# Kernel optimization log

Hardware: AMD Instinct MI355X
Metric: run time of the kernel (lower is better)

Reference implementation:

```python
import jax, jax.numpy as jnp
import numpy as np

# --- configuration (matches init_kwargs / input_specs) ---
B = 8            # point clouds per batch
N_PER = 4096     # points per cloud
RATIO = 0.25
M_PER = int(N_PER * RATIO)
K = 64           # max_num_neighbors (hard-coded in source)
R = 0.2          # ball-query radius
C_IN = 64
DIMS = [C_IN + 3, 128, 128, 256]  # local_nn MLP dims (x_j || pos_j - pos_i)


def setup_inputs() -> dict:
    key = jax.random.key(0)
    ks = jax.random.split(key, 8)
    N = B * N_PER
    x = jax.random.normal(ks[0], (N, C_IN), jnp.float32)
    pos = jax.random.uniform(ks[1], (N, 3), jnp.float32)   # unit cube -> r=0.2 meaningful
    batch = jnp.repeat(jnp.arange(B), N_PER)               # sorted cloud ids
    params = {}
    for i, (din, dout) in enumerate(zip(DIMS[:-1], DIMS[1:])):
        params[f"W{i+1}"] = jax.random.normal(ks[2 + i], (din, dout), jnp.float32) / np.sqrt(din)
        params[f"b{i+1}"] = jnp.zeros((dout,), jnp.float32)
    return {"x": x, "pos": pos, "batch": batch, **params}


def _fps(pos, m):
    """Farthest point sampling on one cloud. pos: [n,3] -> [m] int32 indices.
    Deterministic start at index 0 (torch_geometric uses a random start)."""
    n = pos.shape[0]

    def step(carry, _):
        d, cur = carry
        dist = jnp.sum((pos - pos[cur]) ** 2, axis=-1)
        d = jnp.minimum(d, dist)
        nxt = jnp.argmax(d).astype(jnp.int32)
        return (d, nxt), cur

    init = (jnp.full((n,), jnp.inf, pos.dtype), jnp.int32(0))
    (_, _), idx = jax.lax.scan(step, init, None, length=m)
    return idx  # [m]


def _sa_one(x, pos, W1, b1, W2, b2, W3, b3):
    """One cloud: fps -> radius ball query (<=K nearest within R) -> PointConv (max aggr)."""
    idx = _fps(pos, M_PER)                 # [m]
    q = pos[idx]                           # [m,3] centroids
    d2 = jnp.sum((q[:, None, :] - pos[None, :, :]) ** 2, axis=-1)  # [m,n]
    negd, nbr = jax.lax.top_k(-d2, K)      # K nearest candidates per centroid
    valid = (-negd) <= R * R               # inside the radius ball (self always valid)
    rel = pos[nbr] - q[:, None, :]         # [m,K,3]  pos_j - pos_i
    h = jnp.concatenate([x[nbr], rel], axis=-1)   # [m,K,C+3]
    h = jax.nn.relu(h @ W1 + b1)
    h = jax.nn.relu(h @ W2 + b2)
    h = jax.nn.relu(h @ W3 + b3)           # [m,K,256]
    h = jnp.where(valid[..., None], h, -jnp.inf)
    out = jnp.max(h, axis=1)               # max aggregation over neighbors
    out = jnp.where(jnp.any(valid, axis=1)[..., None], out, 0.0)
    return out, idx


def reference(x, pos, batch, W1, b1, W2, b2, W3, b3):
    xb = x.reshape(B, N_PER, C_IN)
    pb = pos.reshape(B, N_PER, 3)
    out, idx = jax.vmap(lambda xc, pc: _sa_one(xc, pc, W1, b1, W2, b2, W3, b3))(xb, pb)
    pos_out = jnp.take_along_axis(pb, idx[..., None], axis=1).reshape(B * M_PER, 3)
    batch_out = jnp.repeat(jnp.arange(B), M_PER)
    return out.reshape(B * M_PER, DIMS[-1]), pos_out, batch_out
```

## Files before the change

### kernel.cpp

```cpp
#include <hip/hip_runtime.h>


#define NB 8
#define NP 4096
#define MP 1024
#define NC 8192
#define CIN 64
#define D1 128
#define D2 128
#define D3 256
#define CAP 512

static constexpr float R2F = 0.04f;

typedef _Float16 f16;
typedef _Float16 half8 __attribute__((ext_vector_type(8)));
typedef float floatx4 __attribute__((ext_vector_type(4)));
typedef unsigned long long u64;

#define OUT1 ((size_t)NC * D3)
#define OUT2 (OUT1 + (size_t)NC * 3)

template<int CTRL>
__device__ __forceinline__ float dppmax(float v) {
  const int iv = __builtin_bit_cast(int, v);
  const int sh = __builtin_amdgcn_update_dpp(iv, iv, CTRL, 0xf, 0xf, false);
  return fmaxf(v, __builtin_bit_cast(float, sh));
}

struct FpsS { float ldspos[NP * 3]; u64 pkey[2][4]; int cidx[MP]; };
struct PkS  { float wl[CIN * D1]; float xl[32 * CIN]; };

__launch_bounds__(256)
__global__ void front_kernel(const float* __restrict__ pos, const float* __restrict__ x,
                             const float* __restrict__ W1, const float* __restrict__ b1,
                             const float* __restrict__ W2, const float* __restrict__ W3,
                             float* __restrict__ qpos, f16* __restrict__ P,
                             f16* __restrict__ W2t, f16* __restrict__ W3t,
                             float* __restrict__ W1b, float* __restrict__ dout) {
  __shared__ __align__(16) char raw[sizeof(FpsS)];
  const int bid = blockIdx.x;
  const int t = threadIdx.x;

  if (bid < NB) {
    FpsS& S = *reinterpret_cast<FpsS*>(raw);
    const int b = bid;
    const int lane = t & 63, wv = t >> 6;
    for (int e = t; e < NP * 3; e += 256) S.ldspos[e] = pos[(size_t)b * NP * 3 + e];
    __syncthreads();
    float px[16], py[16], pz[16], d[16];
    #pragma unroll
    for (int i = 0; i < 16; ++i) {
      const int p = t * 16 + i;
      px[i] = S.ldspos[p * 3 + 0]; py[i] = S.ldspos[p * 3 + 1]; pz[i] = S.ldspos[p * 3 + 2];
      d[i] = INFINITY;
    }
    int g = 0;
    for (int step = 0; step < MP; ++step) {
      if (t == 0) S.cidx[step] = g;
      const float cx = S.ldspos[g * 3 + 0], cy = S.ldspos[g * 3 + 1], cz = S.ldspos[g * 3 + 2];
      float lv = -1.0f;
      #pragma unroll
      for (int i = 0; i < 16; ++i) {
        const float dx = __fsub_rn(px[i], cx);
        const float dy = __fsub_rn(py[i], cy);
        const float dz = __fsub_rn(pz[i], cz);
        const float nd = __fadd_rn(__fadd_rn(__fmul_rn(dx, dx), __fmul_rn(dy, dy)),
                                   __fmul_rn(dz, dz));
        d[i] = fminf(d[i], nd);
        lv = fmaxf(lv, d[i]);
      }
      int li = 15;
      #pragma unroll
      for (int i = 14; i >= 0; --i) li = (d[i] == lv) ? i : li;
      float wm = lv;
      wm = dppmax<0xB1>(wm);
      wm = dppmax<0x4E>(wm);
      wm = dppmax<0x141>(wm);
      wm = dppmax<0x140>(wm);
      wm = dppmax<0x142>(wm);
      wm = dppmax<0x143>(wm);
      const float M = __builtin_bit_cast(float,
          __builtin_amdgcn_readlane(__builtin_bit_cast(int, wm), 63));
      const u64 bal = __ballot(lv == M);
      const int Ls = (int)__builtin_ctzll(bal);
      const int sli = __builtin_amdgcn_readlane(li, Ls);
      const int gw = ((wv << 6) + Ls) * 16 + sli;
      if (lane == 0)
        S.pkey[step & 1][wv] = ((u64)__float_as_uint(M) << 32) | (unsigned int)~gw;
      __syncthreads();
      u64 best = S.pkey[step & 1][0];
      #pragma unroll
      for (int w = 1; w < 4; ++w) {
        const u64 o = S.pkey[step & 1][w];
        best = o > best ? o : best;
      }
      g = (int)~(unsigned int)best;
    }
    __syncthreads();
    for (int s = t; s < MP; s += 256) {
      const int ci = (b << 10) + s;
      const int p = S.cidx[s];
      const float cx = S.ldspos[p * 3 + 0], cy = S.ldspos[p * 3 + 1], cz = S.ldspos[p * 3 + 2];
      qpos[ci * 3 + 0] = cx; qpos[ci * 3 + 1] = cy; qpos[ci * 3 + 2] = cz;
      dout[OUT1 + (size_t)ci * 3 + 0] = cx;
      dout[OUT1 + (size_t)ci * 3 + 1] = cy;
      dout[OUT1 + (size_t)ci * 3 + 2] = cz;
      dout[OUT2 + ci] = (float)b;
    }
  } else if (bid < NB + 1024) {
    PkS& S = *reinterpret_cast<PkS*>(raw);
    const int r0 = (bid - NB) * 32;
    for (int e = t; e < CIN * D1; e += 256) S.wl[e] = W1[e];
    for (int e = t; e < 32 * CIN; e += 256)
      S.xl[e] = x[(size_t)(r0 + (e >> 6)) * CIN + (e & 63)];
    __syncthreads();
    const int c = t & 127;
    const int rh = t >> 7;
    const float bc = b1[c];
    for (int rr = 0; rr < 32; rr += 2) {
      const int r = rr + rh;
      float acc = bc;
      #pragma unroll
      for (int k = 0; k < CIN; ++k) acc = __fmaf_rn(S.xl[r * CIN + k], S.wl[k * D1 + c], acc);
      P[(size_t)(r0 + r) * D1 + c] = (f16)acc;
    }
  } else {
    const int stride = 64 * 256;
    const int i = (bid - (NB + 1024)) * 256 + t;
    for (int e = i; e < D1 * D2; e += stride) {
      int c = e >> 7, k = e & 127;
      W2t[c * 128 + k] = (f16)W2[k * D2 + c];
    }
    for (int e = i; e < D2 * D3; e += stride) {
      int c = e >> 7, k = e & 127;
      W3t[c * 128 + k] = (f16)W3[k * D3 + c];
    }
    for (int e = i; e < 3 * D1; e += stride) W1b[e] = W1[64 * D1 + e];
  }
}

__launch_bounds__(256)
__global__ void ballq_kernel(const float* __restrict__ pos, const float* __restrict__ qpos,
                             int* __restrict__ nbr) {
  __shared__ unsigned long long list[4][CAP];
  const int t = threadIdx.x;
  const int wv = t >> 6, lane = t & 63;
  const int ci = blockIdx.x * 4 + wv;
  const int b = ci >> 10;
  const int base = b * NP;
  const float qx = qpos[ci * 3 + 0], qy = qpos[ci * 3 + 1], qz = qpos[ci * 3 + 2];
  int cnt = 0;
  for (int chunk = 0; chunk < NP / 64; ++chunk) {
    const int p = chunk * 64 + lane;
    const float x = pos[(size_t)(base + p) * 3 + 0];
    const float y = pos[(size_t)(base + p) * 3 + 1];
    const float z = pos[(size_t)(base + p) * 3 + 2];
    const float dx = __fsub_rn(qx, x), dy = __fsub_rn(qy, y), dz = __fsub_rn(qz, z);
    const float d2 = __fadd_rn(__fadd_rn(__fmul_rn(dx, dx), __fmul_rn(dy, dy)),
                               __fmul_rn(dz, dz));
    const bool in = d2 <= R2F;
    const unsigned long long mask = __ballot(in);
    if (in) {
      const int slot = cnt + __popcll(mask & ((1ull << lane) - 1ull));
      if (slot < CAP)
        list[wv][slot] = ((unsigned long long)__float_as_uint(d2) << 32) | (unsigned int)p;
    }
    cnt += __popcll(mask);
  }
  const int cntc = cnt < CAP ? cnt : CAP;
  for (int s = cntc + lane; s < CAP; s += 64) list[wv][s] = ~0ull;
  __syncthreads();
  for (int ks = 2; ks <= CAP; ks <<= 1) {
    for (int jj = ks >> 1; jj > 0; jj >>= 1) {
      for (int i = lane; i < CAP; i += 64) {
        const int partner = i ^ jj;
        if (partner > i) {
          const bool up = ((i & ks) == 0);
          const unsigned long long a = list[wv][i], c = list[wv][partner];
          if (up ? (a > c) : (a < c)) { list[wv][i] = c; list[wv][partner] = a; }
        }
      }
      __syncthreads();
    }
  }
  const unsigned long long e = list[wv][lane];
  const int idx = (int)(e & 0xFFFFFFFFull);
  nbr[(ci << 6) + lane] = (lane < cntc) ? idx : -1;
}

__launch_bounds__(256)
__global__ void mlp_kernel(const float* __restrict__ pos, const float* __restrict__ qpos,
                           const int* __restrict__ nbr, const f16* __restrict__ P,
                           const float* __restrict__ W1b, const f16* __restrict__ W2t,
                           const float* __restrict__ b2c, const f16* __restrict__ W3t,
                           const float* __restrict__ b3c, float* __restrict__ out) {
  __shared__ f16 h1s[64 * 128];
  __shared__ f16 h2s[64 * 128];
  const int ci = blockIdx.x;
  const int base = (ci >> 10) << 12;
  const int t = threadIdx.x;
  const int lane = t & 63;
  const int wv = __builtin_amdgcn_readfirstlane((int)(t >> 6));
  const int m = lane & 15, qq = lane >> 4;

  const int j = nbr[(ci << 6) + lane];
  const bool valid = j >= 0;
  const int cnt = __popcll(__ballot(valid));
  const int j0 = __shfl(j, 0);
  const int jjn = valid ? j : (j0 >= 0 ? j0 : 0);

  const float qx = qpos[ci * 3 + 0], qy = qpos[ci * 3 + 1], qz = qpos[ci * 3 + 2];
  const float rx = pos[(size_t)(base + jjn) * 3 + 0] - qx;
  const float ry = pos[(size_t)(base + jjn) * 3 + 1] - qy;
  const float rz = pos[(size_t)(base + jjn) * 3 + 2] - qz;

  {
    const f16* Prow = P + (size_t)(base + jjn) * D1;
    const int r = lane;
    #pragma unroll
    for (int c8 = 0; c8 < 4; ++c8) {
      const int c0 = wv * 32 + c8 * 8;
      const half8 pv = *(const half8*)(Prow + c0);
      half8 hv;
      #pragma unroll
      for (int u = 0; u < 8; ++u) {
        const int c = c0 + u;
        float v = (float)pv[u] + rx * W1b[c] + ry * W1b[128 + c] + rz * W1b[256 + c];
        hv[u] = (f16)fmaxf(v, 0.0f);
      }
      *(half8*)(h1s + r * 128 + (c0 ^ ((r & 7) << 3))) = hv;
    }
  }
  __syncthreads();

  {
    floatx4 acc[2][4];
    #pragma unroll
    for (int cs = 0; cs < 2; ++cs)
      #pragma unroll
      for (int rt = 0; rt < 4; ++rt) acc[cs][rt] = floatx4{0.f, 0.f, 0.f, 0.f};
    #pragma unroll
    for (int ks = 0; ks < 4; ++ks) {
      const int kk = ks * 32 + qq * 8;
      half8 af[4];
      #pragma unroll
      for (int rt = 0; rt < 4; ++rt) {
        const int r = rt * 16 + m;
        af[rt] = *(const half8*)(h1s + r * 128 + (kk ^ ((r & 7) << 3)));
      }
      half8 bf[2];
      #pragma unroll
      for (int cs = 0; cs < 2; ++cs) {
        const int c = (wv * 2 + cs) * 16 + m;
        bf[cs] = *(const half8*)(W2t + (size_t)c * 128 + kk);
      }
      #pragma unroll
      for (int cs = 0; cs < 2; ++cs)
        #pragma unroll
        for (int rt = 0; rt < 4; ++rt)
          acc[cs][rt] = __builtin_amdgcn_mfma_f32_16x16x32_f16(af[rt], bf[cs], acc[cs][rt], 0, 0, 0);
    }
    #pragma unroll
    for (int cs = 0; cs < 2; ++cs) {
      const int c = (wv * 2 + cs) * 16 + m;
      const float bias = b2c[c];
      #pragma unroll
      for (int rt = 0; rt < 4; ++rt) {
        #pragma unroll
        for (int u = 0; u < 4; ++u) {
          const int r = rt * 16 + qq * 4 + u;
          h2s[r * 128 + (c ^ ((r & 7) << 3))] = (f16)fmaxf(acc[cs][rt][u] + bias, 0.0f);
        }
      }
    }
  }
  __syncthreads();

  {
    floatx4 acc[4][4];
    #pragma unroll
    for (int ct = 0; ct < 4; ++ct)
      #pragma unroll
      for (int rt = 0; rt < 4; ++rt) acc[ct][rt] = floatx4{0.f, 0.f, 0.f, 0.f};
    #pragma unroll
    for (int ks = 0; ks < 4; ++ks) {
      const int kk = ks * 32 + qq * 8;
      half8 af[4];
      #pragma unroll
      for (int rt = 0; rt < 4; ++rt) {
        const int r = rt * 16 + m;
        af[rt] = *(const half8*)(h2s + r * 128 + (kk ^ ((r & 7) << 3)));
      }
      half8 bf[4];
      #pragma unroll
      for (int ct = 0; ct < 4; ++ct) {
        const int c = (wv * 4 + ct) * 16 + m;
        bf[ct] = *(const half8*)(W3t + (size_t)c * 128 + kk);
      }
      #pragma unroll
      for (int ct = 0; ct < 4; ++ct)
        #pragma unroll
        for (int rt = 0; rt < 4; ++rt)
          acc[ct][rt] = __builtin_amdgcn_mfma_f32_16x16x32_f16(af[rt], bf[ct], acc[ct][rt], 0, 0, 0);
    }
    #pragma unroll
    for (int ct = 0; ct < 4; ++ct) {
      const int c = (wv * 4 + ct) * 16 + m;
      const float bias = b3c[c];
      float mx = -INFINITY;
      #pragma unroll
      for (int rt = 0; rt < 4; ++rt) {
        #pragma unroll
        for (int u = 0; u < 4; ++u) {
          const int r = rt * 16 + qq * 4 + u;
          float v = fmaxf(acc[ct][rt][u] + bias, 0.0f);
          v = (r < cnt) ? v : -INFINITY;
          mx = fmaxf(mx, v);
        }
      }
      mx = fmaxf(mx, __shfl_xor(mx, 16));
      mx = fmaxf(mx, __shfl_xor(mx, 32));
      mx = (cnt > 0) ? mx : 0.0f;
      if (qq == 0) out[(size_t)ci * D3 + c] = mx;
    }
  }
}

extern "C" void kernel_launch(void* const* d_in, const int* in_sizes, int n_in,
                              void* d_out, int out_size, void* d_ws, size_t ws_size,
                              hipStream_t stream) {
  const float* x   = (const float*)d_in[0];
  const float* pos = (const float*)d_in[1];
  const float* W1 = (const float*)d_in[3];
  const float* b1 = (const float*)d_in[4];
  const float* W2 = (const float*)d_in[5];
  const float* b2 = (const float*)d_in[6];
  const float* W3 = (const float*)d_in[7];
  const float* b3 = (const float*)d_in[8];
  float* out = (float*)d_out;

  char* ws = (char*)d_ws;
  f16*   P    = (f16*)  (ws + 0);
  float* qpos = (float*)(ws + 8388608);
  int*   nbr  = (int*)  (ws + 8486912);
  f16*   W2t  = (f16*)  (ws + 10584064);
  f16*   W3t  = (f16*)  (ws + 10616832);
  float* W1b  = (float*)(ws + 10682368);

  front_kernel<<<NB + 1024 + 64, 256, 0, stream>>>(pos, x, W1, b1, W2, W3,
                                                   qpos, P, W2t, W3t, W1b, out);
  ballq_kernel<<<NC / 4, 256, 0, stream>>>(pos, qpos, nbr);
  mlp_kernel<<<NC, 256, 0, stream>>>(pos, qpos, nbr, P, W1b, W2t, b2, W3t, b3, out);
}
```

Measured before the change: 860.5 us.

## Pack FPS distance math into float2 ops and run ball query one wave per block

The FPS loop now holds point coordinates as float2 pairs so subtraction, multiply and add can lower to packed fp32 instructions, with fp contraction disabled so results stay bit-exact with the reference and the argmax picks the same points. The ball-query kernel moves from four waves per block sharing block-wide barriers to one 64-thread block per centroid. Each bitonic stage then waits only on its own wave instead of the slowest of four. The cost is four times as many blocks, each with a small LDS footprint.

New measurement: 835.9 us. 2.9% less time.

```diff
diff --git a/kernel.cpp b/kernel.cpp
--- a/kernel.cpp
+++ b/kernel.cpp
@@ -16,6 +16,7 @@
 typedef _Float16 f16;
 typedef _Float16 half8 __attribute__((ext_vector_type(8)));
 typedef float floatx4 __attribute__((ext_vector_type(4)));
+typedef float f32x2 __attribute__((ext_vector_type(2)));
 typedef unsigned long long u64;
 
 #define OUT1 ((size_t)NC * D3)
@@ -38,6 +39,7 @@
                              float* __restrict__ qpos, f16* __restrict__ P,
                              f16* __restrict__ W2t, f16* __restrict__ W3t,
                              float* __restrict__ W1b, float* __restrict__ dout) {
+  #pragma clang fp contract(off)
   __shared__ __align__(16) char raw[sizeof(FpsS)];
   const int bid = blockIdx.x;
   const int t = threadIdx.x;
@@ -48,27 +50,32 @@
     const int lane = t & 63, wv = t >> 6;
     for (int e = t; e < NP * 3; e += 256) S.ldspos[e] = pos[(size_t)b * NP * 3 + e];
     __syncthreads();
-    float px[16], py[16], pz[16], d[16];
-    #pragma unroll
-    for (int i = 0; i < 16; ++i) {
-      const int p = t * 16 + i;
-      px[i] = S.ldspos[p * 3 + 0]; py[i] = S.ldspos[p * 3 + 1]; pz[i] = S.ldspos[p * 3 + 2];
-      d[i] = INFINITY;
+    f32x2 px[8], py[8], pz[8];
+    float d[16];
+    #pragma unroll
+    for (int i = 0; i < 8; ++i) {
+      const int p = t * 16 + 2 * i;
+      px[i] = (f32x2){S.ldspos[p * 3 + 0], S.ldspos[p * 3 + 3]};
+      py[i] = (f32x2){S.ldspos[p * 3 + 1], S.ldspos[p * 3 + 4]};
+      pz[i] = (f32x2){S.ldspos[p * 3 + 2], S.ldspos[p * 3 + 5]};
+      d[2 * i] = INFINITY; d[2 * i + 1] = INFINITY;
     }
     int g = 0;
     for (int step = 0; step < MP; ++step) {
       if (t == 0) S.cidx[step] = g;
       const float cx = S.ldspos[g * 3 + 0], cy = S.ldspos[g * 3 + 1], cz = S.ldspos[g * 3 + 2];
+      const f32x2 cx2 = cx, cy2 = cy, cz2 = cz;
       float lv = -1.0f;
       #pragma unroll
-      for (int i = 0; i < 16; ++i) {
-        const float dx = __fsub_rn(px[i], cx);
-        const float dy = __fsub_rn(py[i], cy);
-        const float dz = __fsub_rn(pz[i], cz);
-        const float nd = __fadd_rn(__fadd_rn(__fmul_rn(dx, dx), __fmul_rn(dy, dy)),
-                                   __fmul_rn(dz, dz));
-        d[i] = fminf(d[i], nd);
-        lv = fmaxf(lv, d[i]);
+      for (int i = 0; i < 8; ++i) {
+        const f32x2 dx = px[i] - cx2;
+        const f32x2 dy = py[i] - cy2;
+        const f32x2 dz = pz[i] - cz2;
+        const f32x2 nd = (dx * dx + dy * dy) + dz * dz;
+        d[2 * i]     = fminf(d[2 * i],     nd.x);
+        d[2 * i + 1] = fminf(d[2 * i + 1], nd.y);
+        lv = fmaxf(lv, d[2 * i]);
+        lv = fmaxf(lv, d[2 * i + 1]);
       }
       int li = 15;
       #pragma unroll
@@ -140,13 +147,12 @@
   }
 }
 
-__launch_bounds__(256)
+__launch_bounds__(64)
 __global__ void ballq_kernel(const float* __restrict__ pos, const float* __restrict__ qpos,
                              int* __restrict__ nbr) {
-  __shared__ unsigned long long list[4][CAP];
-  const int t = threadIdx.x;
-  const int wv = t >> 6, lane = t & 63;
-  const int ci = blockIdx.x * 4 + wv;
+  __shared__ unsigned long long list[CAP];
+  const int lane = threadIdx.x;
+  const int ci = blockIdx.x;
   const int b = ci >> 10;
   const int base = b * NP;
   const float qx = qpos[ci * 3 + 0], qy = qpos[ci * 3 + 1], qz = qpos[ci * 3 + 2];
@@ -164,12 +170,12 @@
     if (in) {
       const int slot = cnt + __popcll(mask & ((1ull << lane) - 1ull));
       if (slot < CAP)
-        list[wv][slot] = ((unsigned long long)__float_as_uint(d2) << 32) | (unsigned int)p;
+        list[slot] = ((unsigned long long)__float_as_uint(d2) << 32) | (unsigned int)p;
     }
     cnt += __popcll(mask);
   }
   const int cntc = cnt < CAP ? cnt : CAP;
-  for (int s = cntc + lane; s < CAP; s += 64) list[wv][s] = ~0ull;
+  for (int s = cntc + lane; s < CAP; s += 64) list[s] = ~0ull;
   __syncthreads();
   for (int ks = 2; ks <= CAP; ks <<= 1) {
     for (int jj = ks >> 1; jj > 0; jj >>= 1) {
@@ -177,14 +183,14 @@
         const int partner = i ^ jj;
         if (partner > i) {
           const bool up = ((i & ks) == 0);
-          const unsigned long long a = list[wv][i], c = list[wv][partner];
-          if (up ? (a > c) : (a < c)) { list[wv][i] = c; list[wv][partner] = a; }
+          const unsigned long long a = list[i], c = list[partner];
+          if (up ? (a > c) : (a < c)) { list[i] = c; list[partner] = a; }
         }
       }
       __syncthreads();
     }
   }
-  const unsigned long long e = list[wv][lane];
+  const unsigned long long e = list[lane];
   const int idx = (int)(e & 0xFFFFFFFFull);
   nbr[(ci << 6) + lane] = (lane < cntc) ? idx : -1;
 }
@@ -350,6 +356,6 @@
 
   front_kernel<<<NB + 1024 + 64, 256, 0, stream>>>(pos, x, W1, b1, W2, W3,
                                                    qpos, P, W2t, W3t, W1b, out);
-  ballq_kernel<<<NC / 4, 256, 0, stream>>>(pos, qpos, nbr);
+  ballq_kernel<<<NC, 64, 0, stream>>>(pos, qpos, nbr);
   mlp_kernel<<<NC, 256, 0, stream>>>(pos, qpos, nbr, P, W1b, W2t, b2, W3t, b3, out);
 }
```

## Interleave two FPS clouds per block with packed math; drop ballq block barriers

Applied to the files above, without the earlier changes.

Each FPS block now processes two point clouds together. The two clouds' dependent argmax chains interleave, so they share one __syncthreads per step, and the distance math uses packed two-wide float vectors. Both clouds' positions sit in dynamic shared memory, which is large enough to limit occupancy for the other front_kernel blocks that use the same launch. The ball-query bitonic sort loses its block-wide barriers because each wave sorts only its own list; this relies on intra-wave LDS ordering.

Measured after the change: 1.230 ms. 1.43x slower.

```diff
diff --git a/kernel.cpp b/kernel.cpp
--- a/kernel.cpp
+++ b/kernel.cpp
@@ -16,6 +16,7 @@
 typedef _Float16 f16;
 typedef _Float16 half8 __attribute__((ext_vector_type(8)));
 typedef float floatx4 __attribute__((ext_vector_type(4)));
+typedef float f32x2 __attribute__((ext_vector_type(2)));
 typedef unsigned long long u64;
 
 #define OUT1 ((size_t)NC * D3)
@@ -28,8 +29,12 @@
   return fmaxf(v, __builtin_bit_cast(float, sh));
 }
 
-struct FpsS { float ldspos[NP * 3]; u64 pkey[2][4]; int cidx[MP]; };
-struct PkS  { float wl[CIN * D1]; float xl[32 * CIN]; };
+struct FpsS2 {
+  u64 pkey[2][2][4];
+  int cidx[2][MP];
+  float ldspos[2][NP * 3];
+};
+struct PkS { float wl[CIN * D1]; float xl[32 * CIN]; };
 
 __launch_bounds__(256)
 __global__ void front_kernel(const float* __restrict__ pos, const float* __restrict__ x,
@@ -38,79 +43,100 @@
                              float* __restrict__ qpos, f16* __restrict__ P,
                              f16* __restrict__ W2t, f16* __restrict__ W3t,
                              float* __restrict__ W1b, float* __restrict__ dout) {
-  __shared__ __align__(16) char raw[sizeof(FpsS)];
+  #pragma clang fp contract(off)
+  extern __shared__ __align__(16) char raw[];
   const int bid = blockIdx.x;
   const int t = threadIdx.x;
 
-  if (bid < NB) {
-    FpsS& S = *reinterpret_cast<FpsS*>(raw);
-    const int b = bid;
+  if (bid < NB / 2) {
+    FpsS2& S = *reinterpret_cast<FpsS2*>(raw);
     const int lane = t & 63, wv = t >> 6;
-    for (int e = t; e < NP * 3; e += 256) S.ldspos[e] = pos[(size_t)b * NP * 3 + e];
+    for (int cl = 0; cl < 2; ++cl)
+      for (int e = t; e < NP * 3; e += 256)
+        S.ldspos[cl][e] = pos[(size_t)(bid * 2 + cl) * NP * 3 + e];
     __syncthreads();
-    float px[16], py[16], pz[16], d[16];
-    #pragma unroll
-    for (int i = 0; i < 16; ++i) {
-      const int p = t * 16 + i;
-      px[i] = S.ldspos[p * 3 + 0]; py[i] = S.ldspos[p * 3 + 1]; pz[i] = S.ldspos[p * 3 + 2];
-      d[i] = INFINITY;
-    }
-    int g = 0;
+    f32x2 px[2][8], py[2][8], pz[2][8];
+    float d[2][16];
+    #pragma unroll
+    for (int cl = 0; cl < 2; ++cl)
+      #pragma unroll
+      for (int i = 0; i < 8; ++i) {
+        const int p = t * 16 + 2 * i;
+        px[cl][i] = (f32x2){S.ldspos[cl][p * 3 + 0], S.ldspos[cl][p * 3 + 3]};
+        py[cl][i] = (f32x2){S.ldspos[cl][p * 3 + 1], S.ldspos[cl][p * 3 + 4]};
+        pz[cl][i] = (f32x2){S.ldspos[cl][p * 3 + 2], S.ldspos[cl][p * 3 + 5]};
+        d[cl][2 * i] = INFINITY; d[cl][2 * i + 1] = INFINITY;
+      }
+    int g[2] = {0, 0};
     for (int step = 0; step < MP; ++step) {
-      if (t == 0) S.cidx[step] = g;
-      const float cx = S.ldspos[g * 3 + 0], cy = S.ldspos[g * 3 + 1], cz = S.ldspos[g * 3 + 2];
-      float lv = -1.0f;
-      #pragma unroll
-      for (int i = 0; i < 16; ++i) {
-        const float dx = __fsub_rn(px[i], cx);
-        const float dy = __fsub_rn(py[i], cy);
-        const float dz = __fsub_rn(pz[i], cz);
-        const float nd = __fadd_rn(__fadd_rn(__fmul_rn(dx, dx), __fmul_rn(dy, dy)),
-                                   __fmul_rn(dz, dz));
-        d[i] = fminf(d[i], nd);
-        lv = fmaxf(lv, d[i]);
-      }
-      int li = 15;
-      #pragma unroll
-      for (int i = 14; i >= 0; --i) li = (d[i] == lv) ? i : li;
-      float wm = lv;
-      wm = dppmax<0xB1>(wm);
-      wm = dppmax<0x4E>(wm);
-      wm = dppmax<0x141>(wm);
-      wm = dppmax<0x140>(wm);
-      wm = dppmax<0x142>(wm);
-      wm = dppmax<0x143>(wm);
-      const float M = __builtin_bit_cast(float,
-          __builtin_amdgcn_readlane(__builtin_bit_cast(int, wm), 63));
-      const u64 bal = __ballot(lv == M);
-      const int Ls = (int)__builtin_ctzll(bal);
-      const int sli = __builtin_amdgcn_readlane(li, Ls);
-      const int gw = ((wv << 6) + Ls) * 16 + sli;
-      if (lane == 0)
-        S.pkey[step & 1][wv] = ((u64)__float_as_uint(M) << 32) | (unsigned int)~gw;
+      if (t == 0) { S.cidx[0][step] = g[0]; S.cidx[1][step] = g[1]; }
+      #pragma unroll
+      for (int cl = 0; cl < 2; ++cl) {
+        const float cx = S.ldspos[cl][g[cl] * 3 + 0];
+        const float cy = S.ldspos[cl][g[cl] * 3 + 1];
+        const float cz = S.ldspos[cl][g[cl] * 3 + 2];
+        const f32x2 cx2 = cx, cy2 = cy, cz2 = cz;
+        float lv = -1.0f;
+        #pragma unroll
+        for (int i = 0; i < 8; ++i) {
+          const f32x2 dx = px[cl][i] - cx2;
+          const f32x2 dy = py[cl][i] - cy2;
+          const f32x2 dz = pz[cl][i] - cz2;
+          const f32x2 nd = (dx * dx + dy * dy) + dz * dz;
+          d[cl][2 * i]     = fminf(d[cl][2 * i],     nd.x);
+          d[cl][2 * i + 1] = fminf(d[cl][2 * i + 1], nd.y);
+          lv = fmaxf(lv, d[cl][2 * i]);
+          lv = fmaxf(lv, d[cl][2 * i + 1]);
+        }
+        int li = 15;
+        #pragma unroll
+        for (int i = 14; i >= 0; --i) li = (d[cl][i] == lv) ? i : li;
+        float wm = lv;
+        wm = dppmax<0xB1>(wm);
+        wm = dppmax<0x4E>(wm);
+        wm = dppmax<0x141>(wm);
+        wm = dppmax<0x140>(wm);
+        wm = dppmax<0x142>(wm);
+        wm = dppmax<0x143>(wm);
+        const float M = __builtin_bit_cast(float,
+            __builtin_amdgcn_readlane(__builtin_bit_cast(int, wm), 63));
+        const u64 bal = __ballot(lv == M);
+        const int Ls = (int)__builtin_ctzll(bal);
+        const int sli = __builtin_amdgcn_readlane(li, Ls);
+        const int gw = ((wv << 6) + Ls) * 16 + sli;
+        if (lane == 0)
+          S.pkey[step & 1][cl][wv] = ((u64)__float_as_uint(M) << 32) | (unsigned int)~gw;
+      }
       __syncthreads();
-      u64 best = S.pkey[step & 1][0];
-      #pragma unroll
-      for (int w = 1; w < 4; ++w) {
-        const u64 o = S.pkey[step & 1][w];
-        best = o > best ? o : best;
-      }
-      g = (int)~(unsigned int)best;
+      #pragma unroll
+      for (int cl = 0; cl < 2; ++cl) {
+        u64 best = S.pkey[step & 1][cl][0];
+        #pragma unroll
+        for (int w = 1; w < 4; ++w) {
+          const u64 o = S.pkey[step & 1][cl][w];
+          best = o > best ? o : best;
+        }
+        g[cl] = (int)~(unsigned int)best;
+      }
     }
     __syncthreads();
-    for (int s = t; s < MP; s += 256) {
-      const int ci = (b << 10) + s;
-      const int p = S.cidx[s];
-      const float cx = S.ldspos[p * 3 + 0], cy = S.ldspos[p * 3 + 1], cz = S.ldspos[p * 3 + 2];
+    for (int s = t; s < 2 * MP; s += 256) {
+      const int cl = s >> 10, ss = s & (MP - 1);
+      const int b = bid * 2 + cl;
+      const int ci = (b << 10) + ss;
+      const int p = S.cidx[cl][ss];
+      const float cx = S.ldspos[cl][p * 3 + 0];
+      const float cy = S.ldspos[cl][p * 3 + 1];
+      const float cz = S.ldspos[cl][p * 3 + 2];
       qpos[ci * 3 + 0] = cx; qpos[ci * 3 + 1] = cy; qpos[ci * 3 + 2] = cz;
       dout[OUT1 + (size_t)ci * 3 + 0] = cx;
       dout[OUT1 + (size_t)ci * 3 + 1] = cy;
       dout[OUT1 + (size_t)ci * 3 + 2] = cz;
       dout[OUT2 + ci] = (float)b;
     }
-  } else if (bid < NB + 1024) {
+  } else if (bid < NB / 2 + 1024) {
     PkS& S = *reinterpret_cast<PkS*>(raw);
-    const int r0 = (bid - NB) * 32;
+    const int r0 = (bid - NB / 2) * 32;
     for (int e = t; e < CIN * D1; e += 256) S.wl[e] = W1[e];
     for (int e = t; e < 32 * CIN; e += 256)
       S.xl[e] = x[(size_t)(r0 + (e >> 6)) * CIN + (e & 63)];
@@ -127,7 +153,7 @@
     }
   } else {
     const int stride = 64 * 256;
-    const int i = (bid - (NB + 1024)) * 256 + t;
+    const int i = (bid - (NB / 2 + 1024)) * 256 + t;
     for (int e = i; e < D1 * D2; e += stride) {
       int c = e >> 7, k = e & 127;
       W2t[c * 128 + k] = (f16)W2[k * D2 + c];
@@ -170,7 +196,6 @@
   }
   const int cntc = cnt < CAP ? cnt : CAP;
   for (int s = cntc + lane; s < CAP; s += 64) list[wv][s] = ~0ull;
-  __syncthreads();
   for (int ks = 2; ks <= CAP; ks <<= 1) {
     for (int jj = ks >> 1; jj > 0; jj >>= 1) {
       for (int i = lane; i < CAP; i += 64) {
@@ -181,7 +206,6 @@
           if (up ? (a > c) : (a < c)) { list[wv][i] = c; list[wv][partner] = a; }
         }
       }
-      __syncthreads();
     }
   }
   const unsigned long long e = list[wv][lane];
@@ -348,8 +372,8 @@
   f16*   W3t  = (f16*)  (ws + 10616832);
   float* W1b  = (float*)(ws + 10682368);
 
-  front_kernel<<<NB + 1024 + 64, 256, 0, stream>>>(pos, x, W1, b1, W2, W3,
-                                                   qpos, P, W2t, W3t, W1b, out);
+  front_kernel<<<NB / 2 + 1024 + 64, 256, sizeof(FpsS2), stream>>>(
+      pos, x, W1, b1, W2, W3, qpos, P, W2t, W3t, W1b, out);
   ballq_kernel<<<NC / 4, 256, 0, stream>>>(pos, qpos, nbr);
   mlp_kernel<<<NC, 256, 0, stream>>>(pos, qpos, nbr, P, W1b, W2t, b2, W3t, b3, out);
 }
```
